# Kernel optimization log

Hardware: AMD Instinct MI355X
Metric: run time of the kernel (lower is better)

The kernel has to match this reference:

```python
import jax, jax.numpy as jnp
import numpy as np
import math

B, L, DIM = 128, 192, 512
NTOKEN = 100
MAX_BONDS = 6
MAX_LEN = 192


def _sinusoidal_pe(max_len, dim):
    pos = np.arange(max_len, dtype=np.float32)[:, None]
    div = np.exp(np.arange(0, dim, 2, dtype=np.float32) * (-math.log(10000.0) / dim))
    pe = np.zeros((max_len, dim), dtype=np.float32)
    pe[:, 0::2] = np.sin(pos * div)
    pe[:, 1::2] = np.cos(pos * div)
    return jnp.asarray(pe[:, None, :])  # [max_len, 1, dim]


def setup_inputs() -> dict:
    key = jax.random.key(0)
    ks = jax.random.split(key, 16)
    s = 0.02
    inp = {
        "element": jax.random.randint(ks[0], (B, L), 0, NTOKEN),
        "bond": jax.random.randint(ks[1], (B, L, MAX_BONDS), 0, L),
        "aroma": jax.random.randint(ks[2], (B, L), 0, 2),
        "charge": jax.random.randint(ks[3], (B, L), 0, 6),
        "segment": jax.random.randint(ks[4], (B, L), 0, 30),
        # parameters
        "pe": _sinusoidal_pe(MAX_LEN, DIM),
        "E_elem": jax.random.normal(ks[5], (NTOKEN, DIM), jnp.float32) * s,
        "E_charge": jax.random.normal(ks[6], (13, DIM), jnp.float32) * s,
        "E_aroma": jax.random.normal(ks[7], (2, DIM), jnp.float32) * s,
        "E_seg": jax.random.normal(ks[8], (30, DIM), jnp.float32) * s,
        "W1": jax.random.normal(ks[9], (DIM, 4 * DIM), jnp.float32) * s,
        "b1": jnp.zeros((4 * DIM,), jnp.float32),
        "W2": jax.random.normal(ks[10], (4 * DIM, DIM), jnp.float32) * s,
        "b2": jnp.zeros((DIM,), jnp.float32),
        "W3": jax.random.normal(ks[11], (DIM, 4 * DIM), jnp.float32) * s,
        "b3": jnp.zeros((4 * DIM,), jnp.float32),
        "W4": jax.random.normal(ks[12], (4 * DIM, DIM), jnp.float32) * s,
        "b4": jnp.zeros((DIM,), jnp.float32),
        "W5": jax.random.normal(ks[13], (DIM, DIM), jnp.float32) * s,
        "b5": jnp.zeros((DIM,), jnp.float32),
    }
    return inp


def _mlp(x, W1, b1, W2, b2, W3, b3, W4, b4, W5, b5):
    x = x + jnp.maximum(x @ W1 + b1, 0.0) @ W2 + b2
    x = x + jnp.maximum(x @ W3 + b3, 0.0) @ W4 + b4
    return x @ W5 + b5


def reference(element, bond, aroma, charge, segment, pe,
              E_elem, E_charge, E_aroma, E_seg,
              W1, b1, W2, b2, W3, b3, W4, b4, W5, b5):
    b, l = element.shape
    # embeddings: all [l, b, dim]
    emb = E_elem[element.T]
    emb = emb + pe[:l]                      # [l,1,dim] broadcast (eval: dropout off)
    emb = emb + E_aroma[aroma.T]
    emb = emb + E_charge[charge.T + 6]
    emb = emb + E_seg[segment.T]
    message = _mlp(emb, W1, b1, W2, b2, W3, b3, W4, b4, W5, b5)  # [l,b,dim]
    # bond aggregation: agg[k] = sum_m message[bond[b,k,m]] excluding self-bonds
    # (equivalent to the dense one-hot einsum with the diagonal masked out)
    msg_bld = jnp.transpose(message, (1, 0, 2))          # [b,l,dim]
    g = msg_bld[jnp.arange(b)[:, None, None], bond]      # [b,l,MAX_BONDS,dim]
    mask = (bond != jnp.arange(l)[None, :, None]).astype(message.dtype)
    agg = jnp.einsum('bkmd,bkm->bkd', g, mask)           # [b,l,dim]
    return emb + jnp.transpose(agg, (1, 0, 2))           # [l,b,dim]
```

## Files before the change

### kernel.cpp

```cpp
#include <hip/hip_runtime.h>
#include <cstdint>
#include <cstddef>

typedef unsigned short u16;
typedef unsigned int u32;

typedef unsigned short u16x8 __attribute__((ext_vector_type(8)));
typedef __bf16 bf16x8 __attribute__((ext_vector_type(8)));
typedef float f32x4 __attribute__((ext_vector_type(4)));
typedef float f32x8 __attribute__((ext_vector_type(8)));

#define NB   128
#define NL   192
#define NTOK (NB * NL)
#define DIM  512
#define HID  2048

static __device__ __forceinline__ float bf2f(u16 h) {
    union { u32 u; float f; } v; v.u = ((u32)h) << 16; return v.f;
}
static __device__ __forceinline__ u16 f2bf(float f) {
    union { float f; u32 u; } v; v.f = f;
    u32 u = v.u + 0x7FFF + ((v.u >> 16) & 1);
    return (u16)(u >> 16);
}

__global__ void transpose_f2b(const float* __restrict__ in, u16* __restrict__ out,
                              int K, int N) {
    __shared__ float tile[32][33];
    int tx = threadIdx.x & 31, ty = threadIdx.x >> 5;
    int n0 = blockIdx.x * 32, k0 = blockIdx.y * 32;
#pragma unroll
    for (int i = 0; i < 4; i++)
        tile[ty + i * 8][tx] = in[(size_t)(k0 + ty + i * 8) * N + n0 + tx];
    __syncthreads();
#pragma unroll
    for (int i = 0; i < 4; i++)
        out[(size_t)(n0 + ty + i * 8) * K + k0 + tx] = f2bf(tile[tx][ty + i * 8]);
}

static __device__ __forceinline__ void add8f(float* acc, const float* p) {
    f32x8 v = *(const f32x8*)p;
#pragma unroll
    for (int i = 0; i < 8; i++) acc[i] += v[i];
}

__global__ void embed_kernel(const int* __restrict__ element, const int* __restrict__ aroma,
                             const int* __restrict__ charge, const int* __restrict__ segment,
                             const float* __restrict__ pe, const float* __restrict__ E_elem,
                             const float* __restrict__ E_charge, const float* __restrict__ E_aroma,
                             const float* __restrict__ E_seg,
                             float* __restrict__ emb32, u16* __restrict__ emb16) {
    int t = blockIdx.x * 4 + (threadIdx.x >> 6);
    int lane = threadIdx.x & 63;
    int l = t >> 7, b = t & 127;
    int d = lane * 8;
    int idx = b * NL + l;
    int e = element[idx];
    int a = aroma[idx];
    int c = charge[idx] + 6;
    int s = segment[idx];
    float acc[8] = {0, 0, 0, 0, 0, 0, 0, 0};
    add8f(acc, E_elem  + (size_t)e * DIM + d);
    add8f(acc, pe      + (size_t)l * DIM + d);
    add8f(acc, E_aroma + (size_t)a * DIM + d);
    add8f(acc, E_charge+ (size_t)c * DIM + d);
    add8f(acc, E_seg   + (size_t)s * DIM + d);
    f32x8 o32; u16x8 o16;
#pragma unroll
    for (int i = 0; i < 8; i++) { o32[i] = acc[i]; o16[i] = f2bf(acc[i]); }
    *(f32x8*)(emb32 + (size_t)t * DIM + d) = o32;
    *(u16x8*)(emb16 + (size_t)t * DIM + d) = o16;
}

__global__ __launch_bounds__(512, 2) void gemm_bt(
    const u16* __restrict__ A, const u16* __restrict__ BT,
    const float* __restrict__ bias, const u16* __restrict__ resid16,
    const float* __restrict__ resid32,
    u16* __restrict__ C, int M, int N, int K, int do_relu) {
    __shared__ __align__(16) u16 smem[256 * 264];

    const int tid  = threadIdx.x;
    const int wave = tid >> 6;
    const int lane = tid & 63;

    const int nwg = gridDim.x;
    const int bid = blockIdx.x;
    const int wg  = ((nwg & 7) == 0) ? ((bid & 7) * (nwg >> 3) + (bid >> 3)) : bid;
    const int nt  = N >> 8;
    const int m0  = (wg / nt) * 256;
    const int n0  = (wg % nt) * 256;

    const int wmh = wave >> 2;
    const int wnq = wave & 3;
    const int fr  = lane & 15;
    const int fq  = lane >> 4;
    const int ck0 = ((fq ^ (fr & 7)) * 8);
    const int ck1 = (((4 | fq) ^ (fr & 7)) * 8);

    const int sRow = tid >> 3;
    const int sChk = ((tid & 7) ^ (sRow & 7)) * 8;
    const int ldst = sRow * 64 + (tid & 7) * 8;

    const u16* Asrc = A  + (size_t)(m0 + sRow) * K + sChk;
    const u16* Bsrc = BT + (size_t)(n0 + sRow) * K + sChk;

    f32x4 acc[8][4] = {};

#define GLL(gp, lp) __builtin_amdgcn_global_load_lds(                            \
        (const __attribute__((address_space(1))) void*)(gp),                     \
        (__attribute__((address_space(3))) void*)(lp), 16, 0, 0)
#define STAGE(buf, kt) do {                                                      \
    GLL(Asrc + (size_t)(kt) * 64,                 &smem[(buf)*16384 +        ldst]); \
    GLL(Bsrc + (size_t)(kt) * 64,                 &smem[32768 + (buf)*16384 +        ldst]); \
    GLL(Asrc + (size_t)(kt) * 64 + (size_t) 64*K, &smem[(buf)*16384 +  4096 + ldst]); \
    GLL(Bsrc + (size_t)(kt) * 64 + (size_t) 64*K, &smem[32768 + (buf)*16384 +  4096 + ldst]); \
    GLL(Asrc + (size_t)(kt) * 64 + (size_t)128*K, &smem[(buf)*16384 +  8192 + ldst]); \
    GLL(Bsrc + (size_t)(kt) * 64 + (size_t)128*K, &smem[32768 + (buf)*16384 +  8192 + ldst]); \
    GLL(Asrc + (size_t)(kt) * 64 + (size_t)192*K, &smem[(buf)*16384 + 12288 + ldst]); \
    GLL(Bsrc + (size_t)(kt) * 64 + (size_t)192*K, &smem[32768 + (buf)*16384 + 12288 + ldst]); \
} while (0)

    const int nk = K >> 6;
    STAGE(0, 0);

    for (int t = 0; t < nk; ++t) {
        asm volatile("s_waitcnt vmcnt(0)\n\ts_barrier" ::: "memory");
        if (t + 1 < nk) STAGE((t + 1) & 1, t + 1);

        const u16* Ab = &smem[(t & 1) * 16384];
        const u16* Bb = &smem[32768 + (t & 1) * 16384];
#pragma unroll
        for (int s = 0; s < 2; ++s) {
            const int ck = s ? ck1 : ck0;
            bf16x8 af[8], bg[4];
#pragma unroll
            for (int i = 0; i < 8; ++i)
                af[i] = *(const bf16x8*)(&Ab[(wmh * 128 + i * 16 + fr) * 64 + ck]);
#pragma unroll
            for (int j = 0; j < 4; ++j)
                bg[j] = *(const bf16x8*)(&Bb[(wnq * 64 + j * 16 + fr) * 64 + ck]);

            __builtin_amdgcn_s_setprio(1);
#pragma unroll
            for (int i = 0; i < 8; ++i)
#pragma unroll
                for (int j = 0; j < 4; ++j)
                    acc[i][j] = __builtin_amdgcn_mfma_f32_16x16x32_bf16(
                        af[i], bg[j], acc[i][j], 0, 0, 0);
            __builtin_amdgcn_s_setprio(0);
        }
    }
#undef STAGE
#undef GLL

    __syncthreads();
#define CSTR 264
#pragma unroll
    for (int j = 0; j < 4; j++) {
        int n = n0 + wnq * 64 + j * 16 + fr;
        float bv = bias[n];
#pragma unroll
        for (int i = 0; i < 8; i++) {
#pragma unroll
            for (int r = 0; r < 4; r++) {
                int m = m0 + wmh * 128 + i * 16 + fq * 4 + r;
                float v = acc[i][j][r] + bv;
                if (do_relu) v = fmaxf(v, 0.0f);
                if (resid16) v += bf2f(resid16[(size_t)m * N + n]);
                if (resid32) v += resid32[(size_t)m * N + n];
                smem[(wmh * 128 + i * 16 + fq * 4 + r) * CSTR + wnq * 64 + j * 16 + fr] = f2bf(v);
            }
        }
    }
    __syncthreads();
    {
        const int erow = tid >> 5;
        const int ecol = (tid & 31) * 8;
#pragma unroll
        for (int rr = 0; rr < 16; ++rr) {
            int row = rr * 16 + erow;
            *(u16x8*)(C + (size_t)(m0 + row) * N + n0 + ecol) =
                *(const u16x8*)(&smem[row * CSTR + ecol]);
        }
    }
#undef CSTR
}

__global__ void agg_kernel(const float* __restrict__ emb32, const u16* __restrict__ msg,
                           const int* __restrict__ bond, float* __restrict__ out) {
    int t = blockIdx.x * 4 + (threadIdx.x >> 6);
    int lane = threadIdx.x & 63;
    int l = t >> 7, b = t & 127;
    int d = lane * 8;
    float acc[8];
    {
        f32x8 v = *(const f32x8*)(emb32 + (size_t)t * DIM + d);
#pragma unroll
        for (int i = 0; i < 8; i++) acc[i] = v[i];
    }
    const int* bp = bond + ((size_t)b * NL + l) * 6;
#pragma unroll
    for (int m = 0; m < 6; m++) {
        int j = bp[m];
        if (j != l) {
            u16x8 g = *(const u16x8*)(msg + ((size_t)j * NB + b) * DIM + d);
#pragma unroll
            for (int i = 0; i < 8; i++) acc[i] += bf2f(g[i]);
        }
    }
    f32x8 o;
#pragma unroll
    for (int i = 0; i < 8; i++) o[i] = acc[i];
    *(f32x8*)(out + (size_t)t * DIM + d) = o;
}

extern "C" void kernel_launch(void* const* d_in, const int* in_sizes, int n_in,
                              void* d_out, int out_size, void* d_ws, size_t ws_size,
                              hipStream_t stream) {
    const int* element = (const int*)d_in[0];
    const int* bond    = (const int*)d_in[1];
    const int* aroma   = (const int*)d_in[2];
    const int* charge  = (const int*)d_in[3];
    const int* segment = (const int*)d_in[4];
    const float* pe      = (const float*)d_in[5];
    const float* E_elem  = (const float*)d_in[6];
    const float* E_charge= (const float*)d_in[7];
    const float* E_aroma = (const float*)d_in[8];
    const float* E_seg   = (const float*)d_in[9];
    const float* W1 = (const float*)d_in[10];
    const float* b1 = (const float*)d_in[11];
    const float* W2 = (const float*)d_in[12];
    const float* b2 = (const float*)d_in[13];
    const float* W3 = (const float*)d_in[14];
    const float* b3 = (const float*)d_in[15];
    const float* W4 = (const float*)d_in[16];
    const float* b4 = (const float*)d_in[17];
    const float* W5 = (const float*)d_in[18];
    const float* b5 = (const float*)d_in[19];

    float* emb32 = (float*)d_out;

    char* ws = (char*)d_ws;
    size_t woff = 0;
    auto take = [&](size_t bytes) -> u16* {
        u16* p = (u16*)(ws + woff);
        woff += (bytes + 255) & ~(size_t)255;
        return p;
    };
    u16* W1T = take((size_t)HID * DIM * 2);
    u16* W2T = take((size_t)DIM * HID * 2);
    u16* W3T = take((size_t)HID * DIM * 2);
    u16* W4T = take((size_t)DIM * HID * 2);
    u16* W5T = take((size_t)DIM * DIM * 2);
    u16* emb16 = take((size_t)NTOK * DIM * 2);
    u16* msg   = take((size_t)NTOK * DIM * 2);

    static const int ncs[] = {1, 2, 3, 4, 6, 8, 12, 16, 24, 32, 48, 96};
    int CM = 256;
    for (int nc : ncs) {
        int cm = NTOK / nc;
        if (cm % 256 != 0) continue;
        size_t need = woff + ((size_t)cm * HID * 2 + 256)
                           + ((size_t)cm * DIM * 2 + 256) * 2;
        if (need <= ws_size) { CM = cm; break; }
    }
    u16* hC  = take((size_t)CM * HID * 2);
    u16* xaC = take((size_t)CM * DIM * 2);
    u16* xbC = take((size_t)CM * DIM * 2);

    transpose_f2b<<<dim3(HID / 32, DIM / 32), 256, 0, stream>>>(W1, W1T, DIM, HID);
    transpose_f2b<<<dim3(DIM / 32, HID / 32), 256, 0, stream>>>(W2, W2T, HID, DIM);
    transpose_f2b<<<dim3(HID / 32, DIM / 32), 256, 0, stream>>>(W3, W3T, DIM, HID);
    transpose_f2b<<<dim3(DIM / 32, HID / 32), 256, 0, stream>>>(W4, W4T, HID, DIM);
    transpose_f2b<<<dim3(DIM / 32, DIM / 32), 256, 0, stream>>>(W5, W5T, DIM, DIM);

    embed_kernel<<<NTOK / 4, 256, 0, stream>>>(element, aroma, charge, segment, pe,
                                               E_elem, E_charge, E_aroma, E_seg,
                                               emb32, emb16);

    for (int c0 = 0; c0 < NTOK; c0 += CM) {
        const u16* x16 = emb16 + (size_t)c0 * DIM;
        const float* x32 = emb32 + (size_t)c0 * DIM;
        u16* msgC = msg + (size_t)c0 * DIM;
        int mt = CM / 256;
        gemm_bt<<<dim3(mt * (HID / 256)), 512, 0, stream>>>(x16, W1T, b1, nullptr, nullptr, hC,  CM, HID, DIM, 1);
        gemm_bt<<<dim3(mt * (DIM / 256)), 512, 0, stream>>>(hC,  W2T, b2, nullptr, x32,     xaC, CM, DIM, HID, 0);
        gemm_bt<<<dim3(mt * (HID / 256)), 512, 0, stream>>>(xaC, W3T, b3, nullptr, nullptr, hC,  CM, HID, DIM, 1);
        gemm_bt<<<dim3(mt * (DIM / 256)), 512, 0, stream>>>(hC,  W4T, b4, xaC,    nullptr,  xbC, CM, DIM, HID, 0);
        gemm_bt<<<dim3(mt * (DIM / 256)), 512, 0, stream>>>(xbC, W5T, b5, nullptr, nullptr, msgC, CM, DIM, DIM, 0);
    }

    agg_kernel<<<NTOK / 4, 256, 0, stream>>>(emb32, msg, bond, (float*)d_out);
}
```

Measured before the change: 487.7 us.

## Shrink GEMM tile to 256x128 and add triple-buffered LDS pipeline

Each GEMM block now covers 256x128 instead of 256x256, with eight waves arranged 4x2 over 64x64 sub-tiles. That halves the accumulator registers per wave and doubles the grid size. The K loop becomes triple-buffered, prefetching two stages ahead and waiting with vmcnt(6) so loads for the next stage stay in flight during the MFMAs. The trade-off is lower arithmetic intensity per block (more B-tile reloads of A) and 144KB of LDS per block, which may limit occupancy to one block per CU.

```diff
diff --git a/kernel.cpp b/kernel.cpp
--- a/kernel.cpp
+++ b/kernel.cpp
@@ -78,7 +78,7 @@
     const float* __restrict__ bias, const u16* __restrict__ resid16,
     const float* __restrict__ resid32,
     u16* __restrict__ C, int M, int N, int K, int do_relu) {
-    __shared__ __align__(16) u16 smem[256 * 264];
+    __shared__ __align__(16) u16 smem[73728];
 
     const int tid  = threadIdx.x;
     const int wave = tid >> 6;
@@ -87,12 +87,12 @@
     const int nwg = gridDim.x;
     const int bid = blockIdx.x;
     const int wg  = ((nwg & 7) == 0) ? ((bid & 7) * (nwg >> 3) + (bid >> 3)) : bid;
-    const int nt  = N >> 8;
+    const int nt  = N >> 7;
     const int m0  = (wg / nt) * 256;
-    const int n0  = (wg % nt) * 256;
-
-    const int wmh = wave >> 2;
-    const int wnq = wave & 3;
+    const int n0  = (wg % nt) * 128;
+
+    const int wm  = (wave >> 1) * 64;
+    const int wn  = (wave & 1) * 64;
     const int fr  = lane & 15;
     const int fq  = lane >> 4;
     const int ck0 = ((fq ^ (fr & 7)) * 8);
@@ -105,81 +105,89 @@
     const u16* Asrc = A  + (size_t)(m0 + sRow) * K + sChk;
     const u16* Bsrc = BT + (size_t)(n0 + sRow) * K + sChk;
 
-    f32x4 acc[8][4] = {};
+    f32x4 acc[4][4] = {};
 
 #define GLL(gp, lp) __builtin_amdgcn_global_load_lds(                            \
         (const __attribute__((address_space(1))) void*)(gp),                     \
         (__attribute__((address_space(3))) void*)(lp), 16, 0, 0)
 #define STAGE(buf, kt) do {                                                      \
-    GLL(Asrc + (size_t)(kt) * 64,                 &smem[(buf)*16384 +        ldst]); \
-    GLL(Bsrc + (size_t)(kt) * 64,                 &smem[32768 + (buf)*16384 +        ldst]); \
+    GLL(Asrc + (size_t)(kt) * 64,                 &smem[(buf)*16384 +         ldst]); \
     GLL(Asrc + (size_t)(kt) * 64 + (size_t) 64*K, &smem[(buf)*16384 +  4096 + ldst]); \
-    GLL(Bsrc + (size_t)(kt) * 64 + (size_t) 64*K, &smem[32768 + (buf)*16384 +  4096 + ldst]); \
     GLL(Asrc + (size_t)(kt) * 64 + (size_t)128*K, &smem[(buf)*16384 +  8192 + ldst]); \
-    GLL(Bsrc + (size_t)(kt) * 64 + (size_t)128*K, &smem[32768 + (buf)*16384 +  8192 + ldst]); \
     GLL(Asrc + (size_t)(kt) * 64 + (size_t)192*K, &smem[(buf)*16384 + 12288 + ldst]); \
-    GLL(Bsrc + (size_t)(kt) * 64 + (size_t)192*K, &smem[32768 + (buf)*16384 + 12288 + ldst]); \
+    GLL(Bsrc + (size_t)(kt) * 64,                 &smem[49152 + (buf)*8192 +        ldst]); \
+    GLL(Bsrc + (size_t)(kt) * 64 + (size_t) 64*K, &smem[49152 + (buf)*8192 + 4096 + ldst]); \
 } while (0)
 
     const int nk = K >> 6;
     STAGE(0, 0);
-
+    STAGE(1, 1);
+
+    int bt = 0;
     for (int t = 0; t < nk; ++t) {
-        asm volatile("s_waitcnt vmcnt(0)\n\ts_barrier" ::: "memory");
-        if (t + 1 < nk) STAGE((t + 1) & 1, t + 1);
-
-        const u16* Ab = &smem[(t & 1) * 16384];
-        const u16* Bb = &smem[32768 + (t & 1) * 16384];
+        if (t + 1 < nk)
+            asm volatile("s_waitcnt vmcnt(6)\n\ts_barrier" ::: "memory");
+        else
+            asm volatile("s_waitcnt vmcnt(0)\n\ts_barrier" ::: "memory");
+
+        if (t + 2 < nk) {
+            int nb = bt + 2; if (nb >= 3) nb -= 3;
+            STAGE(nb, t + 2);
+        }
+
+        const u16* Ab = &smem[bt * 16384];
+        const u16* Bb = &smem[49152 + bt * 8192];
 #pragma unroll
         for (int s = 0; s < 2; ++s) {
             const int ck = s ? ck1 : ck0;
-            bf16x8 af[8], bg[4];
-#pragma unroll
-            for (int i = 0; i < 8; ++i)
-                af[i] = *(const bf16x8*)(&Ab[(wmh * 128 + i * 16 + fr) * 64 + ck]);
+            bf16x8 af[4], bg[4];
+#pragma unroll
+            for (int i = 0; i < 4; ++i)
+                af[i] = *(const bf16x8*)(&Ab[(wm + i * 16 + fr) * 64 + ck]);
 #pragma unroll
             for (int j = 0; j < 4; ++j)
-                bg[j] = *(const bf16x8*)(&Bb[(wnq * 64 + j * 16 + fr) * 64 + ck]);
+                bg[j] = *(const bf16x8*)(&Bb[(wn + j * 16 + fr) * 64 + ck]);
 
             __builtin_amdgcn_s_setprio(1);
 #pragma unroll
-            for (int i = 0; i < 8; ++i)
+            for (int i = 0; i < 4; ++i)
 #pragma unroll
                 for (int j = 0; j < 4; ++j)
                     acc[i][j] = __builtin_amdgcn_mfma_f32_16x16x32_bf16(
                         af[i], bg[j], acc[i][j], 0, 0, 0);
             __builtin_amdgcn_s_setprio(0);
         }
+        bt = (bt == 2) ? 0 : bt + 1;
     }
 #undef STAGE
 #undef GLL
 
     __syncthreads();
-#define CSTR 264
+#define CSTR 136
 #pragma unroll
     for (int j = 0; j < 4; j++) {
-        int n = n0 + wnq * 64 + j * 16 + fr;
+        int n = n0 + wn + j * 16 + fr;
         float bv = bias[n];
 #pragma unroll
-        for (int i = 0; i < 8; i++) {
+        for (int i = 0; i < 4; i++) {
 #pragma unroll
             for (int r = 0; r < 4; r++) {
-                int m = m0 + wmh * 128 + i * 16 + fq * 4 + r;
+                int m = m0 + wm + i * 16 + fq * 4 + r;
                 float v = acc[i][j][r] + bv;
                 if (do_relu) v = fmaxf(v, 0.0f);
                 if (resid16) v += bf2f(resid16[(size_t)m * N + n]);
                 if (resid32) v += resid32[(size_t)m * N + n];
-                smem[(wmh * 128 + i * 16 + fq * 4 + r) * CSTR + wnq * 64 + j * 16 + fr] = f2bf(v);
+                smem[(wm + i * 16 + fq * 4 + r) * CSTR + wn + j * 16 + fr] = f2bf(v);
             }
         }
     }
     __syncthreads();
     {
-        const int erow = tid >> 5;
-        const int ecol = (tid & 31) * 8;
-#pragma unroll
-        for (int rr = 0; rr < 16; ++rr) {
-            int row = rr * 16 + erow;
+        const int erow = tid >> 4;
+        const int ecol = (tid & 15) * 8;
+#pragma unroll
+        for (int rr = 0; rr < 8; ++rr) {
+            int row = rr * 32 + erow;
             *(u16x8*)(C + (size_t)(m0 + row) * N + n0 + ecol) =
                 *(const u16x8*)(&smem[row * CSTR + ecol]);
         }
@@ -284,11 +292,11 @@
         const float* x32 = emb32 + (size_t)c0 * DIM;
         u16* msgC = msg + (size_t)c0 * DIM;
         int mt = CM / 256;
-        gemm_bt<<<dim3(mt * (HID / 256)), 512, 0, stream>>>(x16, W1T, b1, nullptr, nullptr, hC,  CM, HID, DIM, 1);
-        gemm_bt<<<dim3(mt * (DIM / 256)), 512, 0, stream>>>(hC,  W2T, b2, nullptr, x32,     xaC, CM, DIM, HID, 0);
-        gemm_bt<<<dim3(mt * (HID / 256)), 512, 0, stream>>>(xaC, W3T, b3, nullptr, nullptr, hC,  CM, HID, DIM, 1);
-        gemm_bt<<<dim3(mt * (DIM / 256)), 512, 0, stream>>>(hC,  W4T, b4, xaC,    nullptr,  xbC, CM, DIM, HID, 0);
-        gemm_bt<<<dim3(mt * (DIM / 256)), 512, 0, stream>>>(xbC, W5T, b5, nullptr, nullptr, msgC, CM, DIM, DIM, 0);
+        gemm_bt<<<dim3(mt * (HID / 128)), 512, 0, stream>>>(x16, W1T, b1, nullptr, nullptr, hC,  CM, HID, DIM, 1);
+        gemm_bt<<<dim3(mt * (DIM / 128)), 512, 0, stream>>>(hC,  W2T, b2, nullptr, x32,     xaC, CM, DIM, HID, 0);
+        gemm_bt<<<dim3(mt * (HID / 128)), 512, 0, stream>>>(xaC, W3T, b3, nullptr, nullptr, hC,  CM, HID, DIM, 1);
+        gemm_bt<<<dim3(mt * (DIM / 128)), 512, 0, stream>>>(hC,  W4T, b4, xaC,    nullptr,  xbC, CM, DIM, HID, 0);
+        gemm_bt<<<dim3(mt * (DIM / 128)), 512, 0, stream>>>(xbC, W5T, b5, nullptr, nullptr, msgC, CM, DIM, DIM, 0);
     }
 
     agg_kernel<<<NTOK / 4, 256, 0, stream>>>(emb32, msg, bond, (float*)d_out);
```

After: 524.6 us. 7.6% more time.

## Restructure GEMM main loop into fine-grained interleaved load/MFMA phases

Applied to the files above, without the earlier changes.

The GEMM main loop is rewritten to process two K-tiles per iteration in four quarter phases. Each phase splits global-to-LDS staging of A and B into half-tile chunks and interleaves them with LDS fragment loads and MFMA groups, using partial vmcnt/lgkmcnt waits and extra barriers. The goal is to hide memory latency behind compute instead of waiting on a full vmcnt(0) every tile. Shared memory is cut to 64K u16 by writing the epilogue in two 128-row halves, which may let two workgroups fit per CU. The trade-off is many more barriers per iteration, and the code assumes K is a multiple of 128.

```diff
diff --git a/kernel.cpp b/kernel.cpp
--- a/kernel.cpp
+++ b/kernel.cpp
@@ -78,7 +78,7 @@
     const float* __restrict__ bias, const u16* __restrict__ resid16,
     const float* __restrict__ resid32,
     u16* __restrict__ C, int M, int N, int K, int do_relu) {
-    __shared__ __align__(16) u16 smem[256 * 264];
+    __shared__ __align__(16) u16 smem[65536];
 
     const int tid  = threadIdx.x;
     const int wave = tid >> 6;
@@ -100,7 +100,7 @@
 
     const int sRow = tid >> 3;
     const int sChk = ((tid & 7) ^ (sRow & 7)) * 8;
-    const int ldst = sRow * 64 + (tid & 7) * 8;
+    const int lin  = sRow * 64 + (tid & 7) * 8;
 
     const u16* Asrc = A  + (size_t)(m0 + sRow) * K + sChk;
     const u16* Bsrc = BT + (size_t)(n0 + sRow) * K + sChk;
@@ -110,81 +110,136 @@
 #define GLL(gp, lp) __builtin_amdgcn_global_load_lds(                            \
         (const __attribute__((address_space(1))) void*)(gp),                     \
         (__attribute__((address_space(3))) void*)(lp), 16, 0, 0)
-#define STAGE(buf, kt) do {                                                      \
-    GLL(Asrc + (size_t)(kt) * 64,                 &smem[(buf)*16384 +        ldst]); \
-    GLL(Bsrc + (size_t)(kt) * 64,                 &smem[32768 + (buf)*16384 +        ldst]); \
-    GLL(Asrc + (size_t)(kt) * 64 + (size_t) 64*K, &smem[(buf)*16384 +  4096 + ldst]); \
-    GLL(Bsrc + (size_t)(kt) * 64 + (size_t) 64*K, &smem[32768 + (buf)*16384 +  4096 + ldst]); \
-    GLL(Asrc + (size_t)(kt) * 64 + (size_t)128*K, &smem[(buf)*16384 +  8192 + ldst]); \
-    GLL(Bsrc + (size_t)(kt) * 64 + (size_t)128*K, &smem[32768 + (buf)*16384 +  8192 + ldst]); \
-    GLL(Asrc + (size_t)(kt) * 64 + (size_t)192*K, &smem[(buf)*16384 + 12288 + ldst]); \
-    GLL(Bsrc + (size_t)(kt) * 64 + (size_t)192*K, &smem[32768 + (buf)*16384 + 12288 + ldst]); \
+#define STG_A(kt, h) do {                                                        \
+    GLL(Asrc + (size_t)(kt)*64 + (size_t)((h)*128     )*K,                       \
+        &smem[((kt)&1)*16384 + ((h)*128     )*64 + lin]);                        \
+    GLL(Asrc + (size_t)(kt)*64 + (size_t)((h)*128 + 64)*K,                       \
+        &smem[((kt)&1)*16384 + ((h)*128 + 64)*64 + lin]);                        \
 } while (0)
-
-    const int nk = K >> 6;
-    STAGE(0, 0);
-
-    for (int t = 0; t < nk; ++t) {
-        asm volatile("s_waitcnt vmcnt(0)\n\ts_barrier" ::: "memory");
-        if (t + 1 < nk) STAGE((t + 1) & 1, t + 1);
-
-        const u16* Ab = &smem[(t & 1) * 16384];
-        const u16* Bb = &smem[32768 + (t & 1) * 16384];
-#pragma unroll
-        for (int s = 0; s < 2; ++s) {
-            const int ck = s ? ck1 : ck0;
-            bf16x8 af[8], bg[4];
-#pragma unroll
-            for (int i = 0; i < 8; ++i)
-                af[i] = *(const bf16x8*)(&Ab[(wmh * 128 + i * 16 + fr) * 64 + ck]);
-#pragma unroll
-            for (int j = 0; j < 4; ++j)
-                bg[j] = *(const bf16x8*)(&Bb[(wnq * 64 + j * 16 + fr) * 64 + ck]);
-
-            __builtin_amdgcn_s_setprio(1);
-#pragma unroll
-            for (int i = 0; i < 8; ++i)
-#pragma unroll
-                for (int j = 0; j < 4; ++j)
-                    acc[i][j] = __builtin_amdgcn_mfma_f32_16x16x32_bf16(
-                        af[i], bg[j], acc[i][j], 0, 0, 0);
-            __builtin_amdgcn_s_setprio(0);
-        }
-    }
-#undef STAGE
+#define STG_B(kt, h) do {                                                        \
+    GLL(Bsrc + (size_t)(kt)*64 + (size_t)((h)*128     )*K,                       \
+        &smem[32768 + ((kt)&1)*16384 + ((h)*128     )*64 + lin]);                \
+    GLL(Bsrc + (size_t)(kt)*64 + (size_t)((h)*128 + 64)*K,                       \
+        &smem[32768 + ((kt)&1)*16384 + ((h)*128 + 64)*64 + lin]);                \
+} while (0)
+
+#define BARRIER() asm volatile("s_barrier" ::: "memory")
+#define LGKM0() do { asm volatile("s_waitcnt lgkmcnt(0)" ::: "memory");          \
+                     __builtin_amdgcn_sched_barrier(0); } while (0)
+
+#define LOAD_BG(Bb) do {                                                         \
+    _Pragma("unroll") for (int j = 0; j < 4; ++j) {                              \
+        bg[j][0] = *(const bf16x8*)&(Bb)[(wnq*64 + j*16 + fr)*64 + ck0];         \
+        bg[j][1] = *(const bf16x8*)&(Bb)[(wnq*64 + j*16 + fr)*64 + ck1];         \
+    } } while (0)
+#define LOAD_AF(Ab, q) do {                                                      \
+    _Pragma("unroll") for (int ii = 0; ii < 2; ++ii) {                           \
+        af[ii][0] = *(const bf16x8*)&(Ab)[(wmh*128 + ((q)*2+ii)*16 + fr)*64 + ck0]; \
+        af[ii][1] = *(const bf16x8*)&(Ab)[(wmh*128 + ((q)*2+ii)*16 + fr)*64 + ck1]; \
+    } } while (0)
+#define MFMA_Q(q) do {                                                           \
+    __builtin_amdgcn_s_setprio(1);                                               \
+    _Pragma("unroll") for (int ii = 0; ii < 2; ++ii)                             \
+    _Pragma("unroll") for (int j = 0; j < 4; ++j) {                              \
+        acc[(q)*2+ii][j] = __builtin_amdgcn_mfma_f32_16x16x32_bf16(              \
+            af[ii][0], bg[j][0], acc[(q)*2+ii][j], 0, 0, 0);                     \
+        acc[(q)*2+ii][j] = __builtin_amdgcn_mfma_f32_16x16x32_bf16(              \
+            af[ii][1], bg[j][1], acc[(q)*2+ii][j], 0, 0, 0);                     \
+    }                                                                            \
+    __builtin_amdgcn_s_setprio(0); } while (0)
+
+    const u16* Ae = &smem[0];
+    const u16* Ao = &smem[16384];
+    const u16* Be = &smem[32768];
+    const u16* Bo = &smem[49152];
+
+    const int nI = K >> 7;
+    STG_A(0, 0); STG_A(0, 1); STG_B(0, 0); STG_B(0, 1);
+    STG_B(1, 0); STG_B(1, 1);
+    asm volatile("s_waitcnt vmcnt(4)\n\ts_barrier" ::: "memory");
+
+    for (int t = 0; t < nI; ++t) {
+        const int k0t = 2 * t;
+        const bool st = (t + 1 < nI);
+        bf16x8 bg[4][2], af[2][2];
+        LOAD_BG(Be); LOAD_AF(Ae, 0);
+        STG_A(k0t + 1, 0);
+        asm volatile("s_waitcnt lgkmcnt(8)" ::: "memory");
+        BARRIER(); LGKM0(); MFMA_Q(0); BARRIER();
+        LOAD_AF(Ae, 1);
+        STG_A(k0t + 1, 1);
+        BARRIER(); LGKM0(); MFMA_Q(1); BARRIER();
+        LOAD_AF(Ae, 2);
+        if (st) STG_B(k0t + 2, 0);
+        BARRIER(); LGKM0(); MFMA_Q(2); BARRIER();
+        LOAD_AF(Ae, 3);
+        if (st) {
+            STG_B(k0t + 2, 1);
+            asm volatile("s_waitcnt vmcnt(4)" ::: "memory");
+        } else {
+            asm volatile("s_waitcnt vmcnt(0)" ::: "memory");
+        }
+        BARRIER(); LGKM0(); MFMA_Q(3); BARRIER();
+        LOAD_BG(Bo); LOAD_AF(Ao, 0);
+        if (st) STG_A(k0t + 2, 0);
+        asm volatile("s_waitcnt lgkmcnt(8)" ::: "memory");
+        BARRIER(); LGKM0(); MFMA_Q(0); BARRIER();
+        LOAD_AF(Ao, 1);
+        if (st) STG_A(k0t + 2, 1);
+        BARRIER(); LGKM0(); MFMA_Q(1); BARRIER();
+        LOAD_AF(Ao, 2);
+        if (st) STG_B(k0t + 3, 0);
+        BARRIER(); LGKM0(); MFMA_Q(2); BARRIER();
+        LOAD_AF(Ao, 3);
+        if (st) {
+            STG_B(k0t + 3, 1);
+            asm volatile("s_waitcnt vmcnt(4)" ::: "memory");
+        }
+        BARRIER(); LGKM0(); MFMA_Q(3); BARRIER();
+    }
+#undef STG_A
+#undef STG_B
 #undef GLL
-
-    __syncthreads();
+#undef LOAD_BG
+#undef LOAD_AF
+#undef MFMA_Q
+
 #define CSTR 264
 #pragma unroll
-    for (int j = 0; j < 4; j++) {
-        int n = n0 + wnq * 64 + j * 16 + fr;
-        float bv = bias[n];
-#pragma unroll
-        for (int i = 0; i < 8; i++) {
-#pragma unroll
-            for (int r = 0; r < 4; r++) {
-                int m = m0 + wmh * 128 + i * 16 + fq * 4 + r;
-                float v = acc[i][j][r] + bv;
-                if (do_relu) v = fmaxf(v, 0.0f);
-                if (resid16) v += bf2f(resid16[(size_t)m * N + n]);
-                if (resid32) v += resid32[(size_t)m * N + n];
-                smem[(wmh * 128 + i * 16 + fq * 4 + r) * CSTR + wnq * 64 + j * 16 + fr] = f2bf(v);
+    for (int h = 0; h < 2; ++h) {
+        __syncthreads();
+        if (wmh == h) {
+#pragma unroll
+            for (int j = 0; j < 4; j++) {
+                int n = n0 + wnq * 64 + j * 16 + fr;
+                float bv = bias[n];
+#pragma unroll
+                for (int i = 0; i < 8; i++) {
+#pragma unroll
+                    for (int r = 0; r < 4; r++) {
+                        int m = m0 + h * 128 + i * 16 + fq * 4 + r;
+                        float v = acc[i][j][r] + bv;
+                        if (do_relu) v = fmaxf(v, 0.0f);
+                        if (resid16) v += bf2f(resid16[(size_t)m * N + n]);
+                        if (resid32) v += resid32[(size_t)m * N + n];
+                        smem[(i * 16 + fq * 4 + r) * CSTR + wnq * 64 + j * 16 + fr] = f2bf(v);
+                    }
+                }
             }
         }
-    }
-    __syncthreads();
-    {
+        __syncthreads();
         const int erow = tid >> 5;
         const int ecol = (tid & 31) * 8;
 #pragma unroll
-        for (int rr = 0; rr < 16; ++rr) {
+        for (int rr = 0; rr < 8; ++rr) {
             int row = rr * 16 + erow;
-            *(u16x8*)(C + (size_t)(m0 + row) * N + n0 + ecol) =
+            *(u16x8*)(C + (size_t)(m0 + h * 128 + row) * N + n0 + ecol) =
                 *(const u16x8*)(&smem[row * CSTR + ecol]);
         }
     }
 #undef CSTR
+#undef BARRIER
+#undef LGKM0
 }
 
 __global__ void agg_kernel(const float* __restrict__ emb32, const u16* __restrict__ msg,
```

After: 581.3 us. +19.2%, slower.

## Store GEMM activations in 256x64 tiled layout for contiguous A-tile loads

Applied to the files above, without the earlier changes.

The embed kernel and the intermediate GEMMs now write bf16 activations in a blocked layout of contiguous 256x64 tiles, and the GEMM A-operand loads read each k-tile as one contiguous 32KB block instead of 256 strided rows. The residual read path is updated to the tiled indexing, and only the final GEMM writes row-major output for the aggregation kernel. This aims to improve DRAM/L2 locality of A loads, at the cost of more complex index math and a strided epilogue write pattern.

```diff
diff --git a/kernel.cpp b/kernel.cpp
--- a/kernel.cpp
+++ b/kernel.cpp
@@ -15,6 +15,7 @@
 #define NTOK (NB * NL)
 #define DIM  512
 #define HID  2048
+
 
 static __device__ __forceinline__ float bf2f(u16 h) {
     union { u32 u; float f; } v; v.u = ((u32)h) << 16; return v.f;
@@ -70,14 +71,15 @@
 #pragma unroll
     for (int i = 0; i < 8; i++) { o32[i] = acc[i]; o16[i] = f2bf(acc[i]); }
     *(f32x8*)(emb32 + (size_t)t * DIM + d) = o32;
-    *(u16x8*)(emb16 + (size_t)t * DIM + d) = o16;
+    size_t ti = ((size_t)(t >> 8) * 8 + (d >> 6)) * 16384 + (size_t)(t & 255) * 64 + (d & 63);
+    *(u16x8*)(emb16 + ti) = o16;
 }
 
 __global__ __launch_bounds__(512, 2) void gemm_bt(
     const u16* __restrict__ A, const u16* __restrict__ BT,
     const float* __restrict__ bias, const u16* __restrict__ resid16,
     const float* __restrict__ resid32,
-    u16* __restrict__ C, int M, int N, int K, int do_relu) {
+    u16* __restrict__ C, int M, int N, int K, int do_relu, int out_tiled) {
     __shared__ __align__(16) u16 smem[256 * 264];
 
     const int tid  = threadIdx.x;
@@ -102,8 +104,8 @@
     const int sChk = ((tid & 7) ^ (sRow & 7)) * 8;
     const int ldst = sRow * 64 + (tid & 7) * 8;
 
-    const u16* Asrc = A  + (size_t)(m0 + sRow) * K + sChk;
-    const u16* Bsrc = BT + (size_t)(n0 + sRow) * K + sChk;
+    const u16* Atile = A + ((size_t)(m0 >> 8) * (K >> 6)) * 16384 + sRow * 64 + sChk;
+    const u16* Bsrc  = BT + (size_t)(n0 + sRow) * K + sChk;
 
     f32x4 acc[8][4] = {};
 
@@ -111,13 +113,13 @@
         (const __attribute__((address_space(1))) void*)(gp),                     \
         (__attribute__((address_space(3))) void*)(lp), 16, 0, 0)
 #define STAGE(buf, kt) do {                                                      \
-    GLL(Asrc + (size_t)(kt) * 64,                 &smem[(buf)*16384 +        ldst]); \
-    GLL(Bsrc + (size_t)(kt) * 64,                 &smem[32768 + (buf)*16384 +        ldst]); \
-    GLL(Asrc + (size_t)(kt) * 64 + (size_t) 64*K, &smem[(buf)*16384 +  4096 + ldst]); \
+    GLL(Atile + (size_t)(kt) * 16384,         &smem[(buf)*16384 +         ldst]); \
+    GLL(Atile + (size_t)(kt) * 16384 +  4096, &smem[(buf)*16384 +  4096 + ldst]); \
+    GLL(Atile + (size_t)(kt) * 16384 +  8192, &smem[(buf)*16384 +  8192 + ldst]); \
+    GLL(Atile + (size_t)(kt) * 16384 + 12288, &smem[(buf)*16384 + 12288 + ldst]); \
+    GLL(Bsrc + (size_t)(kt) * 64,                 &smem[32768 + (buf)*16384 +         ldst]); \
     GLL(Bsrc + (size_t)(kt) * 64 + (size_t) 64*K, &smem[32768 + (buf)*16384 +  4096 + ldst]); \
-    GLL(Asrc + (size_t)(kt) * 64 + (size_t)128*K, &smem[(buf)*16384 +  8192 + ldst]); \
     GLL(Bsrc + (size_t)(kt) * 64 + (size_t)128*K, &smem[32768 + (buf)*16384 +  8192 + ldst]); \
-    GLL(Asrc + (size_t)(kt) * 64 + (size_t)192*K, &smem[(buf)*16384 + 12288 + ldst]); \
     GLL(Bsrc + (size_t)(kt) * 64 + (size_t)192*K, &smem[32768 + (buf)*16384 + 12288 + ldst]); \
 } while (0)
 
@@ -167,14 +169,30 @@
                 int m = m0 + wmh * 128 + i * 16 + fq * 4 + r;
                 float v = acc[i][j][r] + bv;
                 if (do_relu) v = fmaxf(v, 0.0f);
-                if (resid16) v += bf2f(resid16[(size_t)m * N + n]);
+                if (resid16) {
+                    size_t ri = ((size_t)(m >> 8) * (N >> 6) + (n >> 6)) * 16384
+                              + (size_t)(m & 255) * 64 + (n & 63);
+                    v += bf2f(resid16[ri]);
+                }
                 if (resid32) v += resid32[(size_t)m * N + n];
                 smem[(wmh * 128 + i * 16 + fq * 4 + r) * CSTR + wnq * 64 + j * 16 + fr] = f2bf(v);
             }
         }
     }
     __syncthreads();
-    {
+    if (out_tiled) {
+        const size_t tbase = ((size_t)(m0 >> 8) * (N >> 6) + (n0 >> 6)) * 16384;
+        const int rsub = lane >> 3;
+        const int chk  = (lane & 7) * 8;
+#pragma unroll
+        for (int it = 0; it < 16; ++it) {
+            int u = it * 8 + wave;
+            int tc = u >> 5;
+            int row = (u & 31) * 8 + rsub;
+            *(u16x8*)(C + tbase + (size_t)tc * 16384 + row * 64 + chk) =
+                *(const u16x8*)(&smem[row * CSTR + tc * 64 + chk]);
+        }
+    } else {
         const int erow = tid >> 5;
         const int ecol = (tid & 31) * 8;
 #pragma unroll
@@ -284,11 +302,11 @@
         const float* x32 = emb32 + (size_t)c0 * DIM;
         u16* msgC = msg + (size_t)c0 * DIM;
         int mt = CM / 256;
-        gemm_bt<<<dim3(mt * (HID / 256)), 512, 0, stream>>>(x16, W1T, b1, nullptr, nullptr, hC,  CM, HID, DIM, 1);
-        gemm_bt<<<dim3(mt * (DIM / 256)), 512, 0, stream>>>(hC,  W2T, b2, nullptr, x32,     xaC, CM, DIM, HID, 0);
-        gemm_bt<<<dim3(mt * (HID / 256)), 512, 0, stream>>>(xaC, W3T, b3, nullptr, nullptr, hC,  CM, HID, DIM, 1);
-        gemm_bt<<<dim3(mt * (DIM / 256)), 512, 0, stream>>>(hC,  W4T, b4, xaC,    nullptr,  xbC, CM, DIM, HID, 0);
-        gemm_bt<<<dim3(mt * (DIM / 256)), 512, 0, stream>>>(xbC, W5T, b5, nullptr, nullptr, msgC, CM, DIM, DIM, 0);
+        gemm_bt<<<dim3(mt * (HID / 256)), 512, 0, stream>>>(x16, W1T, b1, nullptr, nullptr, hC,  CM, HID, DIM, 1, 1);
+        gemm_bt<<<dim3(mt * (DIM / 256)), 512, 0, stream>>>(hC,  W2T, b2, nullptr, x32,     xaC, CM, DIM, HID, 0, 1);
+        gemm_bt<<<dim3(mt * (HID / 256)), 512, 0, stream>>>(xaC, W3T, b3, nullptr, nullptr, hC,  CM, HID, DIM, 1, 1);
+        gemm_bt<<<dim3(mt * (DIM / 256)), 512, 0, stream>>>(hC,  W4T, b4, xaC,    nullptr,  xbC, CM, DIM, HID, 0, 1);
+        gemm_bt<<<dim3(mt * (DIM / 256)), 512, 0, stream>>>(xbC, W5T, b5, nullptr, nullptr, msgC, CM, DIM, DIM, 0, 0);
     }
 
     agg_kernel<<<NTOK / 4, 256, 0, stream>>>(emb32, msg, bond, (float*)d_out);
```

Result: no change. 488.2 us (+0.1%).
